# Kernel tuning notes

Measured on AMD Instinct MI355X. Metric: run time of the kernel, lower is better.

The kernel has to match this reference:

```python
import jax, jax.numpy as jnp
import numpy as np

N_NODES = 50000
N_GRAPHS = 250
NODES_PER_GRAPH = 200
EDGES_PER_GRAPH = 3200  # avg degree 16
F_IN = 128
EMB = 128
HID = 128
VOCAB = 1000
N_REL = 8


def setup_inputs() -> dict:
    key = jax.random.key(0)
    ks = jax.random.split(key, 16)

    # message: col 0 = discrete token id (stored as float), col 1 = continuous value
    disc = jax.random.randint(ks[0], (N_GRAPHS,), 0, VOCAB).astype(jnp.float32)
    cont = jax.random.normal(ks[1], (N_GRAPHS,), dtype=jnp.float32)
    message = jnp.stack([disc, cont], axis=1)  # [B, 2]

    x = jax.random.normal(ks[2], (N_NODES, F_IN), dtype=jnp.float32)

    # within-graph edges: local indices + per-graph node offset
    offs = (jnp.arange(N_GRAPHS, dtype=jnp.int64) * NODES_PER_GRAPH)[:, None]
    src = (jax.random.randint(ks[3], (N_GRAPHS, EDGES_PER_GRAPH), 0, NODES_PER_GRAPH) + offs).reshape(-1)
    dst = (jax.random.randint(ks[4], (N_GRAPHS, EDGES_PER_GRAPH), 0, NODES_PER_GRAPH) + offs).reshape(-1)
    edge_index = jnp.stack([src, dst], axis=0).astype(jnp.int64)  # [2, E]
    edge_type = jax.random.randint(ks[5], (N_GRAPHS * EDGES_PER_GRAPH,), 0, N_REL).astype(jnp.int64)

    batch = jnp.repeat(jnp.arange(N_GRAPHS, dtype=jnp.int64), NODES_PER_GRAPH)  # [N]

    s = 0.05
    W1 = jax.random.normal(ks[6], (N_REL, F_IN, EMB), dtype=jnp.float32) * s
    root1 = jax.random.normal(ks[7], (F_IN, EMB), dtype=jnp.float32) * s
    b1 = jnp.zeros((EMB,), dtype=jnp.float32)
    W2 = jax.random.normal(ks[8], (N_REL, EMB, EMB), dtype=jnp.float32) * s
    root2 = jax.random.normal(ks[9], (EMB, EMB), dtype=jnp.float32) * s
    b2 = jnp.zeros((EMB,), dtype=jnp.float32)
    embed_table = jax.random.normal(ks[10], (VOCAB, EMB), dtype=jnp.float32) * s
    cont_w = jax.random.normal(ks[11], (1, EMB), dtype=jnp.float32) * s
    cont_b = jnp.zeros((EMB,), dtype=jnp.float32)
    msg_w = jax.random.normal(ks[12], (2 * EMB, HID), dtype=jnp.float32) * s
    msg_b = jnp.zeros((HID,), dtype=jnp.float32)

    return {
        "message": message, "x": x, "edge_index": edge_index, "edge_type": edge_type,
        "batch": batch, "max_nodes": NODES_PER_GRAPH,
        "W1": W1, "root1": root1, "b1": b1, "W2": W2, "root2": root2, "b2": b2,
        "embed_table": embed_table, "cont_w": cont_w, "cont_b": cont_b,
        "msg_w": msg_w, "msg_b": msg_b,
    }


def _rgcn_conv(h, src, dst, edge_type, W, root, b, n_nodes, n_rel):
    # per-node per-relation transform, then gather per edge: avoids [E,F,F] weight gather
    hW = jnp.einsum('nf,rfo->nro', h, W)          # [N, R, O]
    msg = hW[src, edge_type]                       # [E, O]
    # mean aggregation per (dst, relation) as in PyG RGCNConv(aggr='mean')
    key_dr = dst * n_rel + edge_type
    cnt = jax.ops.segment_sum(jnp.ones_like(edge_type, dtype=h.dtype), key_dr,
                              num_segments=n_nodes * n_rel)
    norm = 1.0 / jnp.maximum(cnt[key_dr], 1.0)     # [E]
    agg = jax.ops.segment_sum(msg * norm[:, None], dst, num_segments=n_nodes)  # [N, O]
    return agg + h @ root + b


def reference(message, x, edge_index, edge_type, batch, max_nodes,
              W1, root1, b1, W2, root2, b2,
              embed_table, cont_w, cont_b, msg_w, msg_b):
    n_nodes = x.shape[0]
    n_rel = W1.shape[0]
    n_graphs = message.shape[0]
    src, dst = edge_index[0], edge_index[1]

    # --- RGCN node embeddings (2 layers, ReLU between) ---
    h = _rgcn_conv(x, src, dst, edge_type, W1, root1, b1, n_nodes, n_rel)
    h = jax.nn.relu(h)
    node_emb = _rgcn_conv(h, src, dst, edge_type, W2, root2, b2, n_nodes, n_rel)  # [N, EMB]

    # --- message representation ---
    disc_tok = message[:, 0].astype(jnp.int32)
    disc_emb = embed_table[disc_tok]                                   # [B, EMB]
    cont_emb = jax.nn.relu(message[:, 1:2] @ cont_w + cont_b)          # [B, EMB]
    combined = jnp.concatenate([disc_emb, cont_emb], axis=1)           # [B, 2*EMB]
    message_repr = jax.nn.relu(combined @ msg_w + msg_b)               # [B, HID]

    # --- per-node dot score against its graph's message, padded per graph ---
    scores = jnp.einsum('ne,ne->n', node_emb, message_repr[batch])     # [N]
    counts = jax.ops.segment_sum(jnp.ones((n_nodes,), dtype=jnp.int32), batch,
                                 num_segments=n_graphs)
    start = jnp.cumsum(counts) - counts                                # exclusive cumsum
    pos = jnp.arange(n_nodes) - start[batch]                           # slot within graph
    logits = jnp.full((n_graphs, max_nodes), -jnp.inf, dtype=scores.dtype)
    logits = logits.at[batch, pos].set(scores)
    return logits
```

## Files before the change

kernel.cpp:

```cpp
#include <hip/hip_runtime.h>
#include <stdint.h>

#define G_   250
#define P_   200
#define EPG  3200
#define E_   800000
#define F_   128
#define R_   8
#define HROW 136
#define NKEY (R_ * P_)
#define BSTG (8 * 4 * 64 * 8)

typedef _Float16 f16x8 __attribute__((ext_vector_type(8)));
typedef _Float16 f16x4 __attribute__((ext_vector_type(4)));
typedef float    f32x4 __attribute__((ext_vector_type(4)));
typedef float    f32x16 __attribute__((ext_vector_type(16)));

__global__ __launch_bounds__(256) void k_wstage(const float* __restrict__ W1, const float* __restrict__ root1,
                                                const float* __restrict__ W2, const float* __restrict__ root2,
                                                _Float16* __restrict__ wf) {
  int t = blockIdx.x * 256 + threadIdx.x;
  int n = t & 127;
  int k = (t >> 7) & 127;
  int rl_ = t >> 14;
  int r = rl_ % 9, l = rl_ / 9;
  const float* Wl = (l == 0) ? W1 : W2;
  const float* rt = (l == 0) ? root1 : root2;
  float v = (r < 8) ? Wl[(r * F_ + k) * F_ + n] : rt[k * F_ + n];
  int lane = (n & 31) | (((k >> 3) & 1) << 5);
  int j = k & 7, kt = k >> 4, ntj = n >> 5;
  wf[((((l * 9 + r) * 8 + kt) * 4 + ntj) * 64 + lane) * 8 + j] = (_Float16)v;
}

__global__ __launch_bounds__(512, 1) void k_main(
    const float* __restrict__ x, const int* __restrict__ ei, const int* __restrict__ et,
    const _Float16* __restrict__ wf, const float* __restrict__ b1, const float* __restrict__ b2,
    const float* __restrict__ message, const float* __restrict__ embed,
    const float* __restrict__ cw, const float* __restrict__ cb,
    const float* __restrict__ mw, const float* __restrict__ mb,
    float* __restrict__ out) {
  __shared__ __attribute__((aligned(16))) _Float16 hbuf0[P_ * HROW];
  __shared__ __attribute__((aligned(16))) _Float16 hbuf1[P_ * HROW];
  __shared__ __attribute__((aligned(16))) _Float16 Bstage[BSTG];
  __shared__ unsigned short csrS[EPG];
  __shared__ int offsS[NKEY + 1];
  __shared__ float msgS[F_ + 1];

  int g = blockIdx.x, tid = threadIdx.x;
  int lane = tid & 63, wave = tid >> 6;
  int m32 = lane & 31, kh = lane >> 5;

  int*   Sint = (int*)hbuf1;
  int*   cnt  = Sint;
  int*   cur  = Sint + 1600;
  int*   eRec = Sint + 3200;
  float* comb = (float*)(Sint + 6400);
  float* red  = (float*)(Sint + 6656);

  for (int i = tid; i < P_ * 32; i += 512) {
    int row = i >> 5, c4 = i & 31;
    const float4 v = ((const float4*)x)[(g * P_ + row) * 32 + c4];
    f16x4 pk = { (_Float16)v.x, (_Float16)v.y, (_Float16)v.z, (_Float16)v.w };
    *((f16x4*)&hbuf0[row * HROW + c4 * 4]) = pk;
  }
  for (int i = tid; i < NKEY; i += 512) { cnt[i] = 0; cur[i] = 0; }
  if (tid < F_) {
    int tok = (int)message[g * 2];
    float cont = message[g * 2 + 1];
    comb[tid] = embed[tok * F_ + tid];
    float ce = cont * cw[tid] + cb[tid];
    comb[F_ + tid] = ce > 0.0f ? ce : 0.0f;
  }
  __syncthreads();

  int base = g * EPG, nbase = g * P_;
  if (wave < 6) {
    for (int e = wave * 64 + lane; e < EPG; e += 384) {
      int s = ei[base + e] - nbase;
      int d = ei[E_ + base + e] - nbase;
      int r = et[base + e];
      eRec[e] = s | (d << 8) | (r << 16);
      atomicAdd(&cnt[r * P_ + d], 1);
    }
  } else {
    int col = tid & 127;
    float acc = 0.0f;
#pragma unroll 16
    for (int k2 = 0; k2 < 256; k2++) acc += comb[k2] * mw[k2 * F_ + col];
    red[col] = acc;
  }
  __syncthreads();

  if (wave == 0) {
    int4 vv[8];
    int osum = 0;
    if (lane < 50) {
      const int4* cp = (const int4*)(cnt + lane * 32);
#pragma unroll
      for (int i = 0; i < 8; i++) { vv[i] = cp[i]; osum += vv[i].x + vv[i].y + vv[i].z + vv[i].w; }
    }
    int incl = osum;
#pragma unroll
    for (int d = 1; d < 64; d <<= 1) {
      int t2 = __shfl_up(incl, d, 64);
      if (lane >= d) incl += t2;
    }
    int run = incl - osum;
    if (lane < 50) {
#pragma unroll
      for (int i = 0; i < 8; i++) {
        offsS[lane * 32 + i * 4 + 0] = run; run += vv[i].x;
        offsS[lane * 32 + i * 4 + 1] = run; run += vv[i].y;
        offsS[lane * 32 + i * 4 + 2] = run; run += vv[i].z;
        offsS[lane * 32 + i * 4 + 3] = run; run += vv[i].w;
      }
    }
    if (lane == 0) offsS[NKEY] = EPG;
  } else if (wave == 1) {
    float m0 = mb[lane] + red[lane];
    float m1 = mb[lane + 64] + red[lane + 64];
    m0 = m0 > 0.0f ? m0 : 0.0f;
    m1 = m1 > 0.0f ? m1 : 0.0f;
    msgS[lane] = m0; msgS[lane + 64] = m1;
    float p = m0 * b2[lane] + m1 * b2[lane + 64];
#pragma unroll
    for (int d = 32; d > 0; d >>= 1) p += __shfl_xor(p, d, 64);
    if (lane == 0) msgS[F_] = p;
  }
  __syncthreads();

  for (int e = tid; e < EPG; e += 512) {
    int rec = eRec[e];
    int s = rec & 255, d = (rec >> 8) & 255, r = rec >> 16;
    int key = r * P_ + d;
    int pos = atomicAdd(&cur[key], 1);
    csrS[offsS[key] + pos] = (unsigned short)s;
  }
  __syncthreads();

  int jobBase = wave * 25;
  bool rowAct = (m32 < 25);
  int myD = jobBase + m32;
  int ck = kh * 8;

  for (int l = 0; l < 2; l++) {
    const _Float16* Ap = (l == 0) ? hbuf0 : hbuf1;
    f32x16 acc[4];
#pragma unroll
    for (int nt = 0; nt < 4; nt++)
#pragma unroll
      for (int i = 0; i < 16; i++) acc[nt][i] = 0.0f;
    const _Float16* wl = wf + l * (9 * BSTG);
    for (int r = 0; r < 9; r++) {
      const _Float16* wr = wl + r * BSTG;
      f16x8 st[4];
#pragma unroll
      for (int i = 0; i < 4; i++)
        st[i] = *((const f16x8*)(wr + i * 4096 + tid * 8));
      f16x8 a[8];
      if (r < 8) {
        int o = 0, n = 0;
        if (rowAct) { int key = r * P_ + myD; o = offsS[key]; n = offsS[key + 1] - o; }
        f16x8 z = {0, 0, 0, 0, 0, 0, 0, 0};
#pragma unroll
        for (int kt = 0; kt < 8; kt++) a[kt] = z;
        int t = 0;
        for (; t + 2 <= n; t += 2) {
          int s0 = (int)csrS[o + t];
          int s1 = (int)csrS[o + t + 1];
          const _Float16* hp0 = &Ap[s0 * HROW + ck];
          const _Float16* hp1 = &Ap[s1 * HROW + ck];
          f16x8 u0[8], u1[8];
#pragma unroll
          for (int kt = 0; kt < 8; kt++) u0[kt] = *((const f16x8*)(hp0 + kt * 16));
#pragma unroll
          for (int kt = 0; kt < 8; kt++) u1[kt] = *((const f16x8*)(hp1 + kt * 16));
#pragma unroll
          for (int kt = 0; kt < 8; kt++) a[kt] += u0[kt] + u1[kt];
        }
        if (t < n) {
          int s0 = (int)csrS[o + t];
          const _Float16* hp0 = &Ap[s0 * HROW + ck];
#pragma unroll
          for (int kt = 0; kt < 8; kt++) a[kt] += *((const f16x8*)(hp0 + kt * 16));
        }
        float nf = (n > 0) ? 1.0f / (float)n : 0.0f;
        _Float16 nh = (_Float16)nf;
#pragma unroll
        for (int kt = 0; kt < 8; kt++) a[kt] *= nh;
      } else {
        int rowA = jobBase + (rowAct ? m32 : 24);
        const _Float16* hp = &Ap[rowA * HROW + ck];
#pragma unroll
        for (int kt = 0; kt < 8; kt++) a[kt] = *((const f16x8*)(hp + kt * 16));
      }
#pragma unroll
      for (int i = 0; i < 4; i++)
        *((f16x8*)(Bstage + i * 4096 + tid * 8)) = st[i];
      __syncthreads();
#pragma unroll
      for (int nt = 0; nt < 4; nt++) {
#pragma unroll
        for (int kt = 0; kt < 8; kt++) {
          f16x8 b = *((const f16x8*)&Bstage[((kt * 4 + nt) * 64 + lane) * 8]);
          acc[nt] = __builtin_amdgcn_mfma_f32_32x32x16_f16(a[kt], b, acc[nt], 0, 0, 0);
        }
      }
      __syncthreads();
    }
    if (l == 0) {
#pragma unroll
      for (int nt = 0; nt < 4; nt++) {
        int col = nt * 32 + m32;
        float bias = b1[col];
#pragma unroll
        for (int reg = 0; reg < 16; reg++) {
          int row = (reg & 3) + 8 * (reg >> 2) + 4 * kh;
          if (row < 25) {
            float v = acc[nt][reg] + bias;
            v = v > 0.0f ? v : 0.0f;
            hbuf1[(jobBase + row) * HROW + col] = (_Float16)v;
          }
        }
      }
      __syncthreads();
    } else {
      float db2 = msgS[F_];
#pragma unroll
      for (int reg = 0; reg < 16; reg++) {
        int row = (reg & 3) + 8 * (reg >> 2) + 4 * kh;
        float p = 0.0f;
#pragma unroll
        for (int nt = 0; nt < 4; nt++)
          p += acc[nt][reg] * msgS[nt * 32 + m32];
        p += __shfl_xor(p, 16, 32);
        p += __shfl_xor(p, 8, 32);
        p += __shfl_xor(p, 4, 32);
        p += __shfl_xor(p, 2, 32);
        p += __shfl_xor(p, 1, 32);
        if (m32 == 0 && row < 25)
          out[g * P_ + jobBase + row] = p + db2;
      }
    }
  }
}

extern "C" void kernel_launch(void* const* d_in, const int* in_sizes, int n_in,
                              void* d_out, int out_size, void* d_ws, size_t ws_size,
                              hipStream_t stream) {
  const float* message = (const float*)d_in[0];
  const float* x       = (const float*)d_in[1];
  const int*   ei      = (const int*)d_in[2];
  const int*   et      = (const int*)d_in[3];
  const float* W1      = (const float*)d_in[6];
  const float* root1   = (const float*)d_in[7];
  const float* b1      = (const float*)d_in[8];
  const float* W2      = (const float*)d_in[9];
  const float* root2   = (const float*)d_in[10];
  const float* b2      = (const float*)d_in[11];
  const float* embed   = (const float*)d_in[12];
  const float* cw      = (const float*)d_in[13];
  const float* cb      = (const float*)d_in[14];
  const float* mw      = (const float*)d_in[15];
  const float* mb      = (const float*)d_in[16];

  _Float16* wfrag = (_Float16*)d_ws;
  float*    out   = (float*)d_out;

  hipLaunchKernelGGL(k_wstage, dim3(1152), dim3(256), 0, stream, W1, root1, W2, root2, wfrag);
  hipLaunchKernelGGL(k_main, dim3(G_), dim3(512), 0, stream, x, ei, et, wfrag, b1, b2,
                     message, embed, cw, cb, mw, mb, out);
}
```

Before: 176.5 us.

## Use 1024-thread blocks with 32x64 MFMA tiles and double-buffered weight staging

Raises the block to 16 waves. Each of 14 active waves now computes a 32-row by 64-column output tile instead of one wave handling 25 rows by 128 columns. Weight fragments are double-buffered in LDS with a prefetch of the next relation's slice, so there is one barrier per relation instead of two. The layer-1 output overwrites the single h buffer in place, which frees LDS for the second weight buffer. The cost is that each aggregation gather is done twice (once per column half), some wave slots sit idle, and register pressure may rise with the larger block.

```diff
diff --git a/kernel.cpp b/kernel.cpp
--- a/kernel.cpp
+++ b/kernel.cpp
@@ -9,11 +9,10 @@
 #define R_   8
 #define HROW 136
 #define NKEY (R_ * P_)
-#define BSTG (8 * 4 * 64 * 8)
+#define BSET 16384
 
 typedef _Float16 f16x8 __attribute__((ext_vector_type(8)));
 typedef _Float16 f16x4 __attribute__((ext_vector_type(4)));
-typedef float    f32x4 __attribute__((ext_vector_type(4)));
 typedef float    f32x16 __attribute__((ext_vector_type(16)));
 
 __global__ __launch_bounds__(256) void k_wstage(const float* __restrict__ W1, const float* __restrict__ root1,
@@ -29,41 +28,44 @@
   float v = (r < 8) ? Wl[(r * F_ + k) * F_ + n] : rt[k * F_ + n];
   int lane = (n & 31) | (((k >> 3) & 1) << 5);
   int j = k & 7, kt = k >> 4, ntj = n >> 5;
-  wf[((((l * 9 + r) * 8 + kt) * 4 + ntj) * 64 + lane) * 8 + j] = (_Float16)v;
+  wf[(l * 9 + r) * BSET + ((kt * 4 + ntj) * 64 + lane) * 8 + j] = (_Float16)v;
 }
 
-__global__ __launch_bounds__(512, 1) void k_main(
+__global__ __launch_bounds__(1024) void k_main(
     const float* __restrict__ x, const int* __restrict__ ei, const int* __restrict__ et,
     const _Float16* __restrict__ wf, const float* __restrict__ b1, const float* __restrict__ b2,
     const float* __restrict__ message, const float* __restrict__ embed,
     const float* __restrict__ cw, const float* __restrict__ cb,
     const float* __restrict__ mw, const float* __restrict__ mb,
     float* __restrict__ out) {
-  __shared__ __attribute__((aligned(16))) _Float16 hbuf0[P_ * HROW];
-  __shared__ __attribute__((aligned(16))) _Float16 hbuf1[P_ * HROW];
-  __shared__ __attribute__((aligned(16))) _Float16 Bstage[BSTG];
+  __shared__ __attribute__((aligned(16))) _Float16 hbuf[P_ * HROW];
+  __shared__ __attribute__((aligned(16))) _Float16 Bstage[2][BSET];
   __shared__ unsigned short csrS[EPG];
   __shared__ int offsS[NKEY + 1];
   __shared__ float msgS[F_ + 1];
+  __shared__ float scoreS[2 * P_];
 
   int g = blockIdx.x, tid = threadIdx.x;
   int lane = tid & 63, wave = tid >> 6;
   int m32 = lane & 31, kh = lane >> 5;
 
-  int*   Sint = (int*)hbuf1;
+  f16x8 stA = *((const f16x8*)(wf + tid * 8));
+  f16x8 stB = *((const f16x8*)(wf + 8192 + tid * 8));
+
+  int*   Sint = (int*)Bstage[1];
   int*   cnt  = Sint;
   int*   cur  = Sint + 1600;
   int*   eRec = Sint + 3200;
   float* comb = (float*)(Sint + 6400);
   float* red  = (float*)(Sint + 6656);
 
-  for (int i = tid; i < P_ * 32; i += 512) {
+  for (int i = tid; i < P_ * 32; i += 1024) {
     int row = i >> 5, c4 = i & 31;
     const float4 v = ((const float4*)x)[(g * P_ + row) * 32 + c4];
     f16x4 pk = { (_Float16)v.x, (_Float16)v.y, (_Float16)v.z, (_Float16)v.w };
-    *((f16x4*)&hbuf0[row * HROW + c4 * 4]) = pk;
-  }
-  for (int i = tid; i < NKEY; i += 512) { cnt[i] = 0; cur[i] = 0; }
+    *((f16x4*)&hbuf[row * HROW + c4 * 4]) = pk;
+  }
+  for (int i = tid; i < NKEY; i += 1024) { cnt[i] = 0; cur[i] = 0; }
   if (tid < F_) {
     int tok = (int)message[g * 2];
     float cont = message[g * 2 + 1];
@@ -74,8 +76,8 @@
   __syncthreads();
 
   int base = g * EPG, nbase = g * P_;
-  if (wave < 6) {
-    for (int e = wave * 64 + lane; e < EPG; e += 384) {
+  if (wave < 12) {
+    for (int e = wave * 64 + lane; e < EPG; e += 768) {
       int s = ei[base + e] - nbase;
       int d = ei[E_ + base + e] - nbase;
       int r = et[base + e];
@@ -83,11 +85,12 @@
       atomicAdd(&cnt[r * P_ + d], 1);
     }
   } else {
-    int col = tid & 127;
+    int t2 = tid - 768;
+    int col = t2 & 127, seg = t2 >> 7;
     float acc = 0.0f;
 #pragma unroll 16
-    for (int k2 = 0; k2 < 256; k2++) acc += comb[k2] * mw[k2 * F_ + col];
-    red[col] = acc;
+    for (int k2 = seg * 128; k2 < seg * 128 + 128; k2++) acc += comb[k2] * mw[k2 * F_ + col];
+    red[t2] = acc;
   }
   __syncthreads();
 
@@ -117,8 +120,8 @@
     }
     if (lane == 0) offsS[NKEY] = EPG;
   } else if (wave == 1) {
-    float m0 = mb[lane] + red[lane];
-    float m1 = mb[lane + 64] + red[lane + 64];
+    float m0 = mb[lane] + red[lane] + red[128 + lane];
+    float m1 = mb[lane + 64] + red[lane + 64] + red[192 + lane];
     m0 = m0 > 0.0f ? m0 : 0.0f;
     m1 = m1 > 0.0f ? m1 : 0.0f;
     msgS[lane] = m0; msgS[lane + 64] = m1;
@@ -129,38 +132,42 @@
   }
   __syncthreads();
 
-  for (int e = tid; e < EPG; e += 512) {
+  for (int e = tid; e < EPG; e += 1024) {
     int rec = eRec[e];
     int s = rec & 255, d = (rec >> 8) & 255, r = rec >> 16;
     int key = r * P_ + d;
     int pos = atomicAdd(&cur[key], 1);
     csrS[offsS[key] + pos] = (unsigned short)s;
   }
-  __syncthreads();
-
-  int jobBase = wave * 25;
-  bool rowAct = (m32 < 25);
-  int myD = jobBase + m32;
+  *((f16x8*)(&Bstage[0][tid * 8])) = stA;
+  *((f16x8*)(&Bstage[0][8192 + tid * 8])) = stB;
+  __syncthreads();
+
+  int jobId = wave;
+  bool act = jobId < 14;
+  int mt = jobId >> 1, nh = jobId & 1;
+  int rowM = mt * 32 + m32;
   int ck = kh * 8;
-
-  for (int l = 0; l < 2; l++) {
-    const _Float16* Ap = (l == 0) ? hbuf0 : hbuf1;
-    f32x16 acc[4];
-#pragma unroll
-    for (int nt = 0; nt < 4; nt++)
-#pragma unroll
-      for (int i = 0; i < 16; i++) acc[nt][i] = 0.0f;
-    const _Float16* wl = wf + l * (9 * BSTG);
-    for (int r = 0; r < 9; r++) {
-      const _Float16* wr = wl + r * BSTG;
-      f16x8 st[4];
-#pragma unroll
-      for (int i = 0; i < 4; i++)
-        st[i] = *((const f16x8*)(wr + i * 4096 + tid * 8));
+  float db2 = msgS[F_];
+
+  f32x16 acc0, acc1;
+#pragma unroll
+  for (int i = 0; i < 16; i++) { acc0[i] = 0.0f; acc1[i] = 0.0f; }
+
+  for (int it = 0; it < 18; it++) {
+    f16x8 nA, nB;
+    if (it < 17) {
+      const _Float16* wn = wf + (it + 1) * BSET;
+      nA = *((const f16x8*)(wn + tid * 8));
+      nB = *((const f16x8*)(wn + 8192 + tid * 8));
+    }
+    int r = it - (it >= 9 ? 9 : 0);
+    const _Float16* Bb = Bstage[it & 1];
+    if (act) {
       f16x8 a[8];
       if (r < 8) {
         int o = 0, n = 0;
-        if (rowAct) { int key = r * P_ + myD; o = offsS[key]; n = offsS[key + 1] - o; }
+        if (rowM < P_) { int key = r * P_ + rowM; o = offsS[key]; n = offsS[key + 1] - o; }
         f16x8 z = {0, 0, 0, 0, 0, 0, 0, 0};
 #pragma unroll
         for (int kt = 0; kt < 8; kt++) a[kt] = z;
@@ -168,8 +175,8 @@
         for (; t + 2 <= n; t += 2) {
           int s0 = (int)csrS[o + t];
           int s1 = (int)csrS[o + t + 1];
-          const _Float16* hp0 = &Ap[s0 * HROW + ck];
-          const _Float16* hp1 = &Ap[s1 * HROW + ck];
+          const _Float16* hp0 = &hbuf[s0 * HROW + ck];
+          const _Float16* hp1 = &hbuf[s1 * HROW + ck];
           f16x8 u0[8], u1[8];
 #pragma unroll
           for (int kt = 0; kt < 8; kt++) u0[kt] = *((const f16x8*)(hp0 + kt * 16));
@@ -180,69 +187,75 @@
         }
         if (t < n) {
           int s0 = (int)csrS[o + t];
-          const _Float16* hp0 = &Ap[s0 * HROW + ck];
+          const _Float16* hp0 = &hbuf[s0 * HROW + ck];
 #pragma unroll
           for (int kt = 0; kt < 8; kt++) a[kt] += *((const f16x8*)(hp0 + kt * 16));
         }
         float nf = (n > 0) ? 1.0f / (float)n : 0.0f;
-        _Float16 nh = (_Float16)nf;
-#pragma unroll
-        for (int kt = 0; kt < 8; kt++) a[kt] *= nh;
+        _Float16 nh16 = (_Float16)nf;
+#pragma unroll
+        for (int kt = 0; kt < 8; kt++) a[kt] *= nh16;
       } else {
-        int rowA = jobBase + (rowAct ? m32 : 24);
-        const _Float16* hp = &Ap[rowA * HROW + ck];
+        int rA = rowM < P_ ? rowM : P_ - 1;
+        const _Float16* hp = &hbuf[rA * HROW + ck];
 #pragma unroll
         for (int kt = 0; kt < 8; kt++) a[kt] = *((const f16x8*)(hp + kt * 16));
       }
 #pragma unroll
-      for (int i = 0; i < 4; i++)
-        *((f16x8*)(Bstage + i * 4096 + tid * 8)) = st[i];
-      __syncthreads();
-#pragma unroll
-      for (int nt = 0; nt < 4; nt++) {
-#pragma unroll
-        for (int kt = 0; kt < 8; kt++) {
-          f16x8 b = *((const f16x8*)&Bstage[((kt * 4 + nt) * 64 + lane) * 8]);
-          acc[nt] = __builtin_amdgcn_mfma_f32_32x32x16_f16(a[kt], b, acc[nt], 0, 0, 0);
-        }
-      }
-      __syncthreads();
-    }
-    if (l == 0) {
-#pragma unroll
-      for (int nt = 0; nt < 4; nt++) {
-        int col = nt * 32 + m32;
-        float bias = b1[col];
-#pragma unroll
-        for (int reg = 0; reg < 16; reg++) {
-          int row = (reg & 3) + 8 * (reg >> 2) + 4 * kh;
-          if (row < 25) {
-            float v = acc[nt][reg] + bias;
-            v = v > 0.0f ? v : 0.0f;
-            hbuf1[(jobBase + row) * HROW + col] = (_Float16)v;
+      for (int kt = 0; kt < 8; kt++) {
+        f16x8 b0 = *((const f16x8*)&Bb[((kt * 4 + nh * 2 + 0) * 64 + lane) * 8]);
+        acc0 = __builtin_amdgcn_mfma_f32_32x32x16_f16(a[kt], b0, acc0, 0, 0, 0);
+        f16x8 b1v = *((const f16x8*)&Bb[((kt * 4 + nh * 2 + 1) * 64 + lane) * 8]);
+        acc1 = __builtin_amdgcn_mfma_f32_32x32x16_f16(a[kt], b1v, acc1, 0, 0, 0);
+      }
+    }
+    if (it < 17) {
+      _Float16* Bw = Bstage[(it + 1) & 1];
+      *((f16x8*)(&Bw[tid * 8])) = nA;
+      *((f16x8*)(&Bw[8192 + tid * 8])) = nB;
+    }
+    __syncthreads();
+    if (it == 8) {
+      if (act) {
+#pragma unroll
+        for (int nt2 = 0; nt2 < 2; nt2++) {
+          int col = (nh * 2 + nt2) * 32 + m32;
+          float bias = b1[col];
+          const f32x16& ac = nt2 ? acc1 : acc0;
+#pragma unroll
+          for (int reg = 0; reg < 16; reg++) {
+            int row = mt * 32 + (reg & 3) + 8 * (reg >> 2) + 4 * kh;
+            if (row < P_) {
+              float v = ac[reg] + bias;
+              v = v > 0.0f ? v : 0.0f;
+              hbuf[row * HROW + col] = (_Float16)v;
+            }
           }
         }
       }
       __syncthreads();
-    } else {
-      float db2 = msgS[F_];
-#pragma unroll
-      for (int reg = 0; reg < 16; reg++) {
-        int row = (reg & 3) + 8 * (reg >> 2) + 4 * kh;
-        float p = 0.0f;
-#pragma unroll
-        for (int nt = 0; nt < 4; nt++)
-          p += acc[nt][reg] * msgS[nt * 32 + m32];
-        p += __shfl_xor(p, 16, 32);
-        p += __shfl_xor(p, 8, 32);
-        p += __shfl_xor(p, 4, 32);
-        p += __shfl_xor(p, 2, 32);
-        p += __shfl_xor(p, 1, 32);
-        if (m32 == 0 && row < 25)
-          out[g * P_ + jobBase + row] = p + db2;
-      }
-    }
-  }
+#pragma unroll
+      for (int i = 0; i < 16; i++) { acc0[i] = 0.0f; acc1[i] = 0.0f; }
+    }
+  }
+
+  if (act) {
+#pragma unroll
+    for (int reg = 0; reg < 16; reg++) {
+      int row = mt * 32 + (reg & 3) + 8 * (reg >> 2) + 4 * kh;
+      float p = acc0[reg] * msgS[(nh * 2 + 0) * 32 + m32]
+              + acc1[reg] * msgS[(nh * 2 + 1) * 32 + m32];
+      p += __shfl_xor(p, 16, 32);
+      p += __shfl_xor(p, 8, 32);
+      p += __shfl_xor(p, 4, 32);
+      p += __shfl_xor(p, 2, 32);
+      p += __shfl_xor(p, 1, 32);
+      if (m32 == 0 && row < P_) scoreS[nh * P_ + row] = p;
+    }
+  }
+  __syncthreads();
+  for (int i = tid; i < P_; i += 1024)
+    out[g * P_ + i] = scoreS[i] + scoreS[P_ + i] + db2;
 }
 
 extern "C" void kernel_launch(void* const* d_in, const int* in_sizes, int n_in,
@@ -268,6 +281,6 @@
   float*    out   = (float*)d_out;
 
   hipLaunchKernelGGL(k_wstage, dim3(1152), dim3(256), 0, stream, W1, root1, W2, root2, wfrag);
-  hipLaunchKernelGGL(k_main, dim3(G_), dim3(512), 0, stream, x, ei, et, wfrag, b1, b2,
+  hipLaunchKernelGGL(k_main, dim3(G_), dim3(1024), 0, stream, x, ei, et, wfrag, b1, b2,
                      message, embed, cw, cb, mw, mb, out);
 }
```

Result: slower. 220.9 us (+25.1%).
